# Optimization experiments

Hardware: AMD Instinct MI355X
Metric: run time of the kernel (lower is better)

The kernel has to match this reference:

```python
import jax, jax.numpy as jnp
import numpy as np

NUM_COARSE = 1024

def sqdist(a, b):
    # a: [..., N, 3], b: [..., M, 3] -> [..., N, M] squared euclidean distances
    d = (jnp.sum(a * a, -1)[..., :, None] + jnp.sum(b * b, -1)[..., None, :]
         - 2.0 * jnp.einsum('...nd,...md->...nm', a, b))
    return jnp.maximum(d, 0.0)

def fps_idx(pts, n_samples):
    # pts: [N, 3]; farthest point sampling starting from index 0 (pn2 convention)
    d0 = jnp.sum((pts - pts[0]) ** 2, -1)  # [N]
    def step(dists, _):
        idx = jnp.argmax(dists)
        d = jnp.sum((pts - pts[idx]) ** 2, -1)
        return jnp.minimum(dists, d), idx
    _, idxs = jax.lax.scan(step, d0, None, length=n_samples - 1)
    return jnp.concatenate([jnp.zeros((1,), jnp.int32), idxs.astype(jnp.int32)])

def emd_dist(x, y, eps, iters):
    # x, y: [n, 3] equal-cardinality clouds. Approximate optimal assignment via
    # log-domain entropic OT (eps = regularization, iters = iterations), then
    # per-point squared distance to the matched point (as in the auction EMD kernel).
    n = x.shape[0]
    C = sqdist(x, y)                       # [n, n]
    Cs = jax.lax.stop_gradient(C)          # assignment is a constant wrt grads
    loga = -jnp.log(jnp.float32(n))
    def step(f, _):
        g = -eps * jax.nn.logsumexp((f[:, None] - Cs) / eps + loga, axis=0)
        f = -eps * jax.nn.logsumexp((g[None, :] - Cs) / eps + loga, axis=1)
        return f, None
    f, _ = jax.lax.scan(step, jnp.zeros((n,), Cs.dtype), None, length=iters)
    g = -eps * jax.nn.logsumexp((f[:, None] - Cs) / eps + loga, axis=0)
    assign = jnp.argmax(f[:, None] + g[None, :] - Cs, axis=1)  # [n]
    return jnp.take_along_axis(C, assign[:, None], axis=1)[:, 0]

def chamfer(a, b):
    # a: [B, N, 3], b: [B, M, 3] -> per-point min squared dists ([B,N], [B,M])
    C = sqdist(a, b)
    return jnp.min(C, axis=2), jnp.min(C, axis=1)

def setup_inputs() -> dict:
    key = jax.random.key(0)
    k1, k2, k3 = jax.random.split(key, 3)
    return {
        'output1': jax.random.uniform(k1, (4, NUM_COARSE, 3), jnp.float32),
        'output2': jax.random.uniform(k2, (4, 4096, 3), jnp.float32),
        'gt': jax.random.uniform(k3, (4, 4096, 3), jnp.float32),
        'eps': jnp.float32(0.005),
        'iters': 10,
    }

def reference(output1, output2, gt, eps, iters):
    gt = gt[:, :, :3]
    # --- EMD branch ---
    idx = jax.vmap(lambda p: fps_idx(p, NUM_COARSE))(gt)            # [B, num_coarse]
    gt_fps = jnp.take_along_axis(gt, idx[:, :, None], axis=1)       # [B, num_coarse, 3]
    d1 = jax.vmap(lambda x, y: emd_dist(x, y, eps, iters))(output1, gt_fps)
    emd1 = jnp.sqrt(d1).mean(1)
    d2 = jax.vmap(lambda x, y: emd_dist(x, y, eps, iters))(output2, gt)
    emd2 = jnp.sqrt(d2).mean(1)
    # --- Chamfer branch ---
    d11, d12 = chamfer(gt, output1)
    cd_p1 = (jnp.sqrt(d11).mean(1) + jnp.sqrt(d12).mean(1)) / 2
    cd_t1 = d11.mean(1) + d12.mean(1)
    d21, d22 = chamfer(gt, output2)
    cd_p2 = (jnp.sqrt(d21).mean(1) + jnp.sqrt(d22).mean(1)) / 2
    cd_t2 = d21.mean(1) + d22.mean(1)
    return (output1, output2, emd1, emd2, cd_p1, cd_p2, cd_t1, cd_t2)
```

## Files before the change

### kernel.cpp

```cpp
#include <hip/hip_runtime.h>
#include <math.h>


#define LOG2E 1.4426950408889634f
#define LN2   0.6931471805599453f
#define NEGBIG -3.0e38f

#define SY2(b) ((b) * 512)
#define SYF(b) (2048 + (b) * 16)
#define SYD(b) (2112 + (b) * 16)

typedef float f32x2 __attribute__((ext_vector_type(2)));

#if __has_builtin(__builtin_amdgcn_exp2f)
__device__ __forceinline__ float fexp2(float x) { return __builtin_amdgcn_exp2f(x); }
#else
__device__ __forceinline__ float fexp2(float x) { return exp2f(x); }
#endif

__device__ __forceinline__ float dist_rn(float x, float y, float z,
                                         float qx, float qy, float qz) {
  float dx = __fsub_rn(x, qx), dy = __fsub_rn(y, qy), dz = __fsub_rn(z, qz);
  return __fadd_rn(__fadd_rn(__fmul_rn(dx, dx), __fmul_rn(dy, dy)),
                   __fmul_rn(dz, dz));
}

__device__ __forceinline__ f32x2 dist2_rn(f32x2 x, f32x2 y, f32x2 z,
                                          float qx, float qy, float qz) {
#pragma clang fp contract(off)
  f32x2 dx = x - qx;
  f32x2 dy = y - qy;
  f32x2 dz = z - qz;
  f32x2 xx = dx * dx;
  f32x2 yy = dy * dy;
  f32x2 zz = dz * dz;
  return (xx + yy) + zz;
}

struct FpsS {
  float4 sq[4096];
  unsigned long long xch[4][2];
  int sIdx[64];
};
struct WorkS {
  float4 ldsRow[256];
  float4 ldsC[1024];
  float ldsG2[1024];
  float red[8];
};
struct Emd1S {
  float4 rowsO[1024];
  float4 rowsG[1024];
  float2 part[2][16][64];
  float g2[1024];
  float red[8];
};
union SmemAll {
  FpsS f;
  WorkS w;
  Emd1S e;
  float pad_force_one_block_per_cu[21504];
};

struct UniArgs {
  const float* gt;
  const float* epsP;
  const float4 *o1P4, *o2P4, *gtP4;
  float4* gfP4;
  float2 *gpart2, *fpart2, *apart2;
  unsigned long long* vecT;
  unsigned* sync;
  float* out;
  int NC2, BPB;
};

__device__ __forceinline__ void bar_signal(unsigned* slot, unsigned val) {
  __syncthreads();
  if (threadIdx.x == 0)
    __hip_atomic_store(slot, val, __ATOMIC_RELEASE, __HIP_MEMORY_SCOPE_AGENT);
}
template <int SLP>
__device__ __forceinline__ void bar_waitall(const unsigned* base, int n,
                                            unsigned target) {
  if (threadIdx.x < 64) {
    int l = threadIdx.x;
    for (;;) {
      unsigned v = (l < n)
                       ? __hip_atomic_load(base + l * 16, __ATOMIC_RELAXED,
                                           __HIP_MEMORY_SCOPE_AGENT)
                       : target;
      if (__all((int)(v >= target))) break;
      __builtin_amdgcn_s_sleep(SLP);
    }
    if (l == 0)
      (void)__hip_atomic_load(base, __ATOMIC_ACQUIRE, __HIP_MEMORY_SCOPE_AGENT);
  }
  __syncthreads();
}

__device__ __forceinline__ float blockRedSum(float v, float* red4) {
#pragma unroll
  for (int m = 32; m; m >>= 1) v += __shfl_xor(v, m, 64);
  int lane = threadIdx.x & 63, wid = threadIdx.x >> 6;
  __syncthreads();
  if (lane == 0) red4[wid] = v;
  __syncthreads();
  float s = 0.0f;
  if (threadIdx.x == 0) {
#pragma unroll
    for (int w = 0; w < 4; ++w) s += red4[w];
  }
  return s;
}

__device__ __forceinline__ void poll4(const unsigned long long* v, int tid,
                                      unsigned want, float* w0, float* w1,
                                      float* w2, float* w3) {
  unsigned long long p0, p1, p2, p3;
  for (;;) {
    p0 = __hip_atomic_load(v + tid, __ATOMIC_RELAXED, __HIP_MEMORY_SCOPE_AGENT);
    p1 = __hip_atomic_load(v + tid + 256, __ATOMIC_RELAXED, __HIP_MEMORY_SCOPE_AGENT);
    p2 = __hip_atomic_load(v + tid + 512, __ATOMIC_RELAXED, __HIP_MEMORY_SCOPE_AGENT);
    p3 = __hip_atomic_load(v + tid + 768, __ATOMIC_RELAXED, __HIP_MEMORY_SCOPE_AGENT);
    if ((unsigned)(p0 >> 32) >= want && (unsigned)(p1 >> 32) >= want &&
        (unsigned)(p2 >> 32) >= want && (unsigned)(p3 >> 32) >= want)
      break;
    __builtin_amdgcn_s_sleep(1);
  }
  *w0 = __uint_as_float((unsigned)p0);
  *w1 = __uint_as_float((unsigned)p1);
  *w2 = __uint_as_float((unsigned)p2);
  *w3 = __uint_as_float((unsigned)p3);
}

__device__ __forceinline__ void fma_burst(float* a) {
#pragma unroll
  for (int i = 0; i < 64; ++i) {
    a[0] = fmaf(a[0], 1.0000001f, 1.0e-6f);
    a[1] = fmaf(a[1], 1.0000001f, 1.0e-6f);
    a[2] = fmaf(a[2], 1.0000001f, 1.0e-6f);
    a[3] = fmaf(a[3], 1.0000001f, 1.0e-6f);
  }
}

__device__ void warm_spin(const UniArgs& A) {
  float a[4] = {(float)(threadIdx.x + 1), 1.5f, 2.5f, 3.5f};
  const unsigned* sy = A.sync;
  for (;;) {
    unsigned d0 = __hip_atomic_load(sy + SYD(0), __ATOMIC_RELAXED, __HIP_MEMORY_SCOPE_AGENT);
    unsigned d1 = __hip_atomic_load(sy + SYD(1), __ATOMIC_RELAXED, __HIP_MEMORY_SCOPE_AGENT);
    unsigned d2 = __hip_atomic_load(sy + SYD(2), __ATOMIC_RELAXED, __HIP_MEMORY_SCOPE_AGENT);
    unsigned d3 = __hip_atomic_load(sy + SYD(3), __ATOMIC_RELAXED, __HIP_MEMORY_SCOPE_AGENT);
    if ((d0 & d1 & d2 & d3) != 0u) break;
    fma_burst(a);
  }
  asm volatile("" ::"v"(a[0]), "v"(a[1]), "v"(a[2]), "v"(a[3]));
}

__device__ void warm_wait1(const unsigned* slot, unsigned target) {
  float a[4] = {(float)(threadIdx.x + 1), 1.5f, 2.5f, 3.5f};
  for (;;) {
    unsigned v = __hip_atomic_load(slot, __ATOMIC_RELAXED, __HIP_MEMORY_SCOPE_AGENT);
    if (v >= target) break;
    fma_burst(a);
  }
  asm volatile("" ::"v"(a[0]), "v"(a[1]), "v"(a[2]), "v"(a[3]));
  if (threadIdx.x == 0)
    (void)__hip_atomic_load(slot, __ATOMIC_ACQUIRE, __HIP_MEMORY_SCOPE_AGENT);
  __syncthreads();
}

__global__ __launch_bounds__(256) void prep_kernel(
    const float* __restrict__ o1, const float* __restrict__ o2,
    const float* __restrict__ gt, const float* __restrict__ epsP,
    float4* __restrict__ o1P4, float4* __restrict__ o2P4,
    float4* __restrict__ gtP4) {
  int id = blockIdx.x * 256 + threadIdx.x;
  float eps = *epsP;
  float se = (1.0f / eps) * LOG2E;
  float kxy = sqrtf(se + se);
  const float* src;
  float4* dst;
  if (id < 4096) { src = o1 + 3 * id; dst = o1P4 + id; }
  else if (id < 20480) { int p = id - 4096; src = o2 + 3 * p; dst = o2P4 + p; }
  else { int p = id - 20480; src = gt + 3 * p; dst = gtP4 + p; }
  float x = src[0], y = src[1], z = src[2];
  float xx = x * x + y * y + z * z;
  *dst = make_float4(kxy * x, kxy * y, kxy * z, xx * se);
}

template <int NC>
__device__ __forceinline__ float finalize_w(const float2* __restrict__ part,
                                            int gi, int stride, float nloga2) {
  float2 pp[NC];
#pragma unroll
  for (int c = 0; c < NC; ++c) pp[c] = part[c * stride + gi];
  float m = pp[0].x;
#pragma unroll
  for (int c = 1; c < NC; ++c) m = fmaxf(m, pp[c].x);
  float s = 0.0f;
#pragma unroll
  for (int c = 0; c < NC; ++c) s += pp[c].y * fexp2(pp[c].x - m);
  return nloga2 - (m + __log2f(s));
}

template <int NC>
__device__ void pass2_job(int b, int cb, int ch, const float4* __restrict__ rowP,
                          const float4* __restrict__ colP,
                          const float2* __restrict__ vpart,
                          float2* __restrict__ dst, float4* ldsRow) {
  const int CH = 4096 / NC;
  int tid = threadIdx.x;
  int gj = b * 4096 + cb * 2048 + tid;
  float cx[8], cy[8], cz[8];
#pragma unroll
  for (int c = 0; c < 8; ++c) {
    float4 cp = colP[gj + (c << 8)];
    cx[c] = cp.x; cy[c] = cp.y; cz[c] = cp.z;
  }
  float M[8], S[8];
#pragma unroll
  for (int c = 0; c < 8; ++c) { M[c] = NEGBIG; S[c] = 0.0f; }
  int r0 = ch * CH;
  for (int t0 = 0; t0 < CH; t0 += 256) {
    __syncthreads();
    {
      int gi = b * 4096 + r0 + t0 + tid;
      float4 rp = rowP[gi];
      float w = vpart ? finalize_w<NC>(vpart, gi, 16384, 12.0f) : -rp.w;
      ldsRow[tid] = make_float4(rp.x, rp.y, rp.z, w);
    }
    __syncthreads();
#pragma unroll 1
    for (int r = 0; r < 256; r += 8) {
      float4 q[8];
#pragma unroll
      for (int u = 0; u < 8; ++u) q[u] = ldsRow[r + u];
#pragma unroll
      for (int c = 0; c < 8; ++c) {
        float t[8];
#pragma unroll
        for (int u = 0; u < 8; ++u)
          t[u] = fmaf(cx[c], q[u].x, fmaf(cy[c], q[u].y, fmaf(cz[c], q[u].z, q[u].w)));
        float cm = fmaxf(fmaxf(fmaxf(t[0], t[1]), fmaxf(t[2], t[3])),
                         fmaxf(fmaxf(t[4], t[5]), fmaxf(t[6], t[7])));
        float nM = fmaxf(M[c], cm);
        float s8 = ((fexp2(t[0] - nM) + fexp2(t[1] - nM)) +
                    (fexp2(t[2] - nM) + fexp2(t[3] - nM))) +
                   ((fexp2(t[4] - nM) + fexp2(t[5] - nM)) +
                    (fexp2(t[6] - nM) + fexp2(t[7] - nM)));
        S[c] = fmaf(S[c], fexp2(M[c] - nM), s8);
        M[c] = nM;
      }
    }
  }
#pragma unroll
  for (int c = 0; c < 8; ++c)
    dst[ch * 16384 + gj + (c << 8)] = make_float2(M[c], S[c]);
}

__device__ void cham_job(const float4* __restrict__ aP, const float4* __restrict__ bP,
                         int Na, int Nb, float* outP, float* outT,
                         float scaleP, float scaleT, int b, int rb,
                         WorkS& w, const float* epsP) {
  int tid = threadIdx.x;
  int i0 = rb * 512 + tid, i1 = i0 + 256;
  float4 a0 = aP[b * Na + i0], a1 = aP[b * Na + i1];
  float m0 = 3.0e38f, m1 = 3.0e38f;
  for (int t0 = 0; t0 < Nb; t0 += 1024) {
    __syncthreads();
    for (int t = tid; t < 1024; t += 256) w.ldsC[t] = bP[b * Nb + t0 + t];
    __syncthreads();
#pragma unroll 4
    for (int t = 0; t < 1024; ++t) {
      float4 q = w.ldsC[t];
      float c0 = fmaf(-a0.z, q.z, fmaf(-a0.y, q.y, fmaf(-a0.x, q.x, q.w + a0.w)));
      float c1 = fmaf(-a1.z, q.z, fmaf(-a1.y, q.y, fmaf(-a1.x, q.x, q.w + a1.w)));
      m0 = fminf(m0, c0);
      m1 = fminf(m1, c1);
    }
  }
  float eps = *epsP;
  float inv_se = eps * LN2;
  float d0 = fmaxf(0.0f, m0 * inv_se), d1 = fmaxf(0.0f, m1 * inv_se);
  float s1 = blockRedSum(sqrtf(d0) + sqrtf(d1), w.red);
  float s2 = blockRedSum(d0 + d1, w.red);
  if (tid == 0) {
    atomicAdd(outP, s1 * scaleP);
    atomicAdd(outT, s2 * scaleT);
  }
}

__device__ void chamfer_worker(int g, const UniArgs& A, WorkS& w) {
  for (int cj = g; cj < 104; cj += 88) {
    if (cj < 32) {
      cham_job(A.gtP4, A.o2P4, 4096, 4096, A.out + 61452 + (cj >> 3),
               A.out + 61460 + (cj >> 3), 1.0f / 8192.0f, 1.0f / 4096.0f,
               cj >> 3, cj & 7, w, A.epsP);
    } else if (cj < 64) {
      int j = cj - 32;
      cham_job(A.o2P4, A.gtP4, 4096, 4096, A.out + 61452 + (j >> 3),
               A.out + 61460 + (j >> 3), 1.0f / 8192.0f, 1.0f / 4096.0f,
               j >> 3, j & 7, w, A.epsP);
    } else if (cj < 96) {
      int j = cj - 64;
      cham_job(A.gtP4, A.o1P4, 4096, 1024, A.out + 61448 + (j >> 3),
               A.out + 61456 + (j >> 3), 1.0f / 8192.0f, 1.0f / 4096.0f,
               j >> 3, j & 7, w, A.epsP);
    } else {
      int j = cj - 96;
      cham_job(A.o1P4, A.gtP4, 1024, 4096, A.out + 61448 + (j >> 1),
               A.out + 61456 + (j >> 1), 1.0f / 2048.0f, 1.0f / 1024.0f,
               j >> 1, j & 1, w, A.epsP);
    }
  }
}

template <int NC>
__device__ void assign2_job(int b, int cc, int rb, const UniArgs& A, WorkS& w) {
  int tid = threadIdx.x;
  __syncthreads();
  for (int t = tid; t < 1024; t += 256) {
    int gjc = b * 4096 + cc * 1024 + t;
    float wv = finalize_w<NC>(A.gpart2, gjc, 16384, 12.0f);
    float4 qp = A.gtP4[gjc];
    w.ldsC[t] = make_float4(qp.x, qp.y, qp.z, wv);
    w.ldsG2[t] = wv + qp.w;
  }
  __syncthreads();
#pragma unroll
  for (int rr = 0; rr < 2; ++rr) {
    int gi = b * 4096 + rb * 512 + (rr << 8) + tid;
    float4 rp = A.o2P4[gi];
    float rx = rp.x, ry = rp.y, rz = rp.z, xw = rp.w;
    float bW = NEGBIG;
    int bj = 0;
    for (int t = 0; t < 1024; ++t) {
      float4 q = w.ldsC[t];
      float W = fmaf(rz, q.z, fmaf(ry, q.y, fmaf(rx, q.x, q.w - xw)));
      W = fminf(W, w.ldsG2[t]);
      if (W > bW) { bW = W; bj = cc * 1024 + t; }
    }
    A.apart2[cc * 16384 + gi] = make_float2(bW, __int_as_float(bj));
  }
}

__device__ void combine2_job(int b, int rb, const UniArgs& A, WorkS& w) {
  int tid = threadIdx.x;
  int gi = b * 4096 + (rb << 8) + tid;
  float bW = NEGBIG;
  int bj = 0;
#pragma unroll
  for (int c = 0; c < 4; ++c) {
    float2 p = A.apart2[c * 16384 + gi];
    if (p.x > bW) { bW = p.x; bj = __float_as_int(p.y); }
  }
  float eps = *A.epsP;
  float inv_se = eps * LN2;
  float4 rp = A.o2P4[gi];
  float4 qp = A.gtP4[b * 4096 + bj];
  float dotp = rp.x * qp.x + rp.y * qp.y + rp.z * qp.z;
  float d = fmaxf(0.0f, (rp.w + qp.w - dotp) * inv_se);
  float s = blockRedSum(sqrtf(d), w.red);
  if (tid == 0) atomicAdd(A.out + 61444 + b, s * (1.0f / 4096.0f));
}

__device__ void fps_role(const UniArgs& A, int b, FpsS& f) {
  int tid = threadIdx.x;
  const float* base = A.gt + b * 12288;
  for (int t = tid; t < 4096; t += 256) {
    float x = base[3 * t], y = base[3 * t + 1], z = base[3 * t + 2];
    f.sq[t] = make_float4(x, y, z, x * x + y * y + z * z);
  }
  if (tid < 8) ((unsigned long long*)f.xch)[tid] = 0ull;
  if (tid == 0) f.sIdx[0] = 0;
  __syncthreads();
  float eps = *A.epsP;
  float se = (1.0f / eps) * LOG2E;
  float kxy = sqrtf(se + se);
  float4 p0 = f.sq[0];
  f32x2 PX[8], PY[8], PZ[8];
  float d[16];
#pragma unroll
  for (int k = 0; k < 16; ++k) {
    float4 p = f.sq[tid + (k << 8)];
    PX[k >> 1][k & 1] = p.x;
    PY[k >> 1][k & 1] = p.y;
    PZ[k >> 1][k & 1] = p.z;
    d[k] = dist_rn(p.x, p.y, p.z, p0.x, p0.y, p0.z);
  }
  int lane = tid & 63, w = tid >> 6;
  float qx = p0.x, qy = p0.y, qz = p0.z;
  unsigned long long* xmine = &f.xch[w][0];

#define DPPSTEP(C)                                                             \
  {                                                                            \
    unsigned ov = (unsigned)__builtin_amdgcn_update_dpp(0, (int)bvu, C, 0xf,  \
                                                        0xf, true);           \
    int oi = __builtin_amdgcn_update_dpp(0, bi, C, 0xf, 0xf, true);           \
    bool t = (ov > bvu) || ((ov == bvu) && ((unsigned)oi < (unsigned)bi));    \
    bvu = t ? ov : bvu;                                                        \
    bi = t ? oi : bi;                                                          \
  }
#define XCOMB(G)                                                               \
  {                                                                            \
    unsigned _v = (unsigned)((G) >> 32);                                       \
    int _i = (int)((unsigned)(G) & 0xFFFu);                                    \
    if (_v > bv2 || (_v == bv2 && _i < bi2)) { bv2 = _v; bi2 = _i; }          \
  }

#pragma unroll 1
  for (int s = 1; s < 1024; ++s) {
    if ((s & 63) == 0 && tid < 64) {
      int idx = f.sIdx[tid];
      float4 p = f.sq[idx];
      A.gfP4[(b << 10) + (s - 64) + tid] =
          make_float4(kxy * p.x, kxy * p.y, kxy * p.z, p.w * se);
    }
    float tv[8]; int ti[8];
#pragma unroll
    for (int i = 0; i < 8; ++i) {
      f32x2 nn = dist2_rn(PX[i], PY[i], PZ[i], qx, qy, qz);
      float n0 = fminf(d[2 * i], nn[0]);
      float n1 = fminf(d[2 * i + 1], nn[1]);
      d[2 * i] = n0;
      d[2 * i + 1] = n1;
      bool t = n1 > n0;
      tv[i] = t ? n1 : n0;
      ti[i] = tid + ((t ? (2 * i + 1) : (2 * i)) << 8);
    }
    float uv[4]; int ui[4];
#pragma unroll
    for (int i = 0; i < 4; ++i) {
      bool t = tv[2 * i + 1] > tv[2 * i];
      uv[i] = t ? tv[2 * i + 1] : tv[2 * i];
      ui[i] = t ? ti[2 * i + 1] : ti[2 * i];
    }
    bool tA = uv[1] > uv[0];
    float vA = tA ? uv[1] : uv[0]; int iA = tA ? ui[1] : ui[0];
    bool tB = uv[3] > uv[2];
    float vB = tB ? uv[3] : uv[2]; int iB = tB ? ui[3] : ui[2];
    bool tC = vB > vA;
    float bv = tC ? vB : vA; int bi = tC ? iB : iA;
    unsigned bvu = __float_as_uint(bv);
    DPPSTEP(0xB1)
    DPPSTEP(0x4E)
    DPPSTEP(0x141)
    DPPSTEP(0x140)
    unsigned r0v = (unsigned)__builtin_amdgcn_readlane((int)bvu, 0);
    int r0i = __builtin_amdgcn_readlane(bi, 0);
    unsigned r1v = (unsigned)__builtin_amdgcn_readlane((int)bvu, 16);
    int r1i = __builtin_amdgcn_readlane(bi, 16);
    unsigned r2v = (unsigned)__builtin_amdgcn_readlane((int)bvu, 32);
    int r2i = __builtin_amdgcn_readlane(bi, 32);
    unsigned r3v = (unsigned)__builtin_amdgcn_readlane((int)bvu, 48);
    int r3i = __builtin_amdgcn_readlane(bi, 48);
    bool tP = (r1v > r0v) || (r1v == r0v && r1i < r0i);
    unsigned pv = tP ? r1v : r0v; int pi = tP ? r1i : r0i;
    bool tQ = (r3v > r2v) || (r3v == r2v && r3i < r2i);
    unsigned qv = tQ ? r3v : r2v; int qi = tQ ? r3i : r2i;
    bool tR = (qv > pv) || (qv == pv && qi < pi);
    unsigned wv = tR ? qv : pv; int wi = tR ? qi : pi;
    int par = s & 1;
    unsigned tagw = (unsigned)(s & 1023);
    unsigned long long mine = ((unsigned long long)wv << 32) |
                              ((unsigned long long)tagw << 16) |
                              (unsigned long long)(unsigned)wi;
    if (lane == 0)
      __hip_atomic_store(xmine + par, mine, __ATOMIC_RELAXED,
                         __HIP_MEMORY_SCOPE_WORKGROUP);
    float4 mq = f.sq[wi];
    unsigned long long g1, g2, g3;
    for (;;) {
      g1 = __hip_atomic_load(&f.xch[(w + 1) & 3][par], __ATOMIC_RELAXED,
                             __HIP_MEMORY_SCOPE_WORKGROUP);
      g2 = __hip_atomic_load(&f.xch[(w + 2) & 3][par], __ATOMIC_RELAXED,
                             __HIP_MEMORY_SCOPE_WORKGROUP);
      g3 = __hip_atomic_load(&f.xch[(w + 3) & 3][par], __ATOMIC_RELAXED,
                             __HIP_MEMORY_SCOPE_WORKGROUP);
      if ((((unsigned)(g1 >> 16) & 1023u) == tagw) &
          (((unsigned)(g2 >> 16) & 1023u) == tagw) &
          (((unsigned)(g3 >> 16) & 1023u) == tagw))
        break;
    }
    unsigned bv2 = wv; int bi2 = wi;
    XCOMB(g1) XCOMB(g2) XCOMB(g3)
    float4 q;
    if (bv2 == wv && bi2 == wi) q = mq;
    else q = f.sq[bi2];
    qx = q.x; qy = q.y; qz = q.z;
    if (tid == 0) f.sIdx[s & 63] = bi2;
  }
#undef DPPSTEP
#undef XCOMB
  if (tid < 64) {
    int idx = f.sIdx[tid];
    float4 p = f.sq[idx];
    A.gfP4[(b << 10) + 960 + tid] =
        make_float4(kxy * p.x, kxy * p.y, kxy * p.z, p.w * se);
  }
  bar_signal(A.sync + SYF(b), 1u);
}

__device__ void emd1_role(int eb, int chunk, const UniArgs& A, Emd1S& m) {
  int tid = threadIdx.x;
  warm_wait1(A.sync + SYF(eb), 1u);
  for (int t = tid; t < 1024; t += 256) {
    float4 p = A.o1P4[eb * 1024 + t];
    m.rowsO[t] = make_float4(p.x, p.y, p.z, -p.w);
    m.rowsG[t] = A.gfP4[eb * 1024 + t];
  }
  int lane = tid & 63, rl = tid >> 6;
  int col = chunk * 64 + lane;
  float4 cG = A.gfP4[eb * 1024 + col];
  float4 cO = A.o1P4[eb * 1024 + col];
  unsigned long long* gv = A.vecT + (eb << 10);
  unsigned long long* fv = A.vecT + 4096 + (eb << 10);
  __syncthreads();

  for (int s = 1; s <= 21; ++s) {
    int odd = s & 1, par = s & 1;
    if (s >= 2) {
      const unsigned long long* v = odd ? fv : gv;
      float4* rows = odd ? m.rowsO : m.rowsG;
      unsigned want = (unsigned)(s - 1);
      int rbase = rl * 256 + lane;
      unsigned long long p0, p1, p2, p3;
      for (;;) {
        p0 = __hip_atomic_load(v + rbase, __ATOMIC_RELAXED, __HIP_MEMORY_SCOPE_AGENT);
        p1 = __hip_atomic_load(v + rbase + 64, __ATOMIC_RELAXED, __HIP_MEMORY_SCOPE_AGENT);
        p2 = __hip_atomic_load(v + rbase + 128, __ATOMIC_RELAXED, __HIP_MEMORY_SCOPE_AGENT);
        p3 = __hip_atomic_load(v + rbase + 192, __ATOMIC_RELAXED, __HIP_MEMORY_SCOPE_AGENT);
        if ((unsigned)(p0 >> 32) >= want && (unsigned)(p1 >> 32) >= want &&
            (unsigned)(p2 >> 32) >= want && (unsigned)(p3 >> 32) >= want)
          break;
        __builtin_amdgcn_s_sleep(1);
      }
      rows[rbase].w = __uint_as_float((unsigned)p0);
      rows[rbase + 64].w = __uint_as_float((unsigned)p1);
      rows[rbase + 128].w = __uint_as_float((unsigned)p2);
      rows[rbase + 192].w = __uint_as_float((unsigned)p3);
    }
    const float4* rows = odd ? m.rowsO : m.rowsG;
    float cx = odd ? cG.x : cO.x;
    float cy = odd ? cG.y : cO.y;
    float cz = odd ? cG.z : cO.z;
#pragma unroll 1
    for (int k = 0; k < 4; ++k) {
      int ch = rl * 4 + k;
      float M = NEGBIG, S = 0.0f;
      int r0 = ch * 64;
#pragma unroll 1
      for (int r = 0; r < 64; r += 8) {
        float4 qq[8];
#pragma unroll
        for (int u = 0; u < 8; ++u) qq[u] = rows[r0 + r + u];
        float t8[8];
#pragma unroll
        for (int u = 0; u < 8; ++u)
          t8[u] = fmaf(cx, qq[u].x, fmaf(cy, qq[u].y, fmaf(cz, qq[u].z, qq[u].w)));
        float cm = fmaxf(fmaxf(fmaxf(t8[0], t8[1]), fmaxf(t8[2], t8[3])),
                         fmaxf(fmaxf(t8[4], t8[5]), fmaxf(t8[6], t8[7])));
        float nM = fmaxf(M, cm);
        float s8 = ((fexp2(t8[0] - nM) + fexp2(t8[1] - nM)) +
                    (fexp2(t8[2] - nM) + fexp2(t8[3] - nM))) +
                   ((fexp2(t8[4] - nM) + fexp2(t8[5] - nM)) +
                    (fexp2(t8[6] - nM) + fexp2(t8[7] - nM)));
        S = fmaf(S, fexp2(M - nM), s8);
        M = nM;
      }
      m.part[par][ch][lane] = make_float2(M, S);
    }
    __syncthreads();
    if (tid < 64) {
      float2 pp[16];
#pragma unroll
      for (int c = 0; c < 16; ++c) pp[c] = m.part[par][c][tid];
      float mm = pp[0].x;
#pragma unroll
      for (int c = 1; c < 16; ++c) mm = fmaxf(mm, pp[c].x);
      float ss = 0.0f;
#pragma unroll
      for (int c = 0; c < 16; ++c) ss += pp[c].y * fexp2(pp[c].x - mm);
      float wq = 10.0f - (mm + __log2f(ss));
      unsigned long long pk = ((unsigned long long)(unsigned)s << 32) |
                              (unsigned long long)__float_as_uint(wq);
      __hip_atomic_store((odd ? gv : fv) + col, pk, __ATOMIC_RELAXED,
                         __HIP_MEMORY_SCOPE_AGENT);
    }
  }
  __syncthreads();

  {
    float w0, w1, w2, w3;
    poll4(gv, tid, 21u, &w0, &w1, &w2, &w3);
    float4 qp0 = A.gfP4[eb * 1024 + tid];
    float4 qp1 = A.gfP4[eb * 1024 + tid + 256];
    float4 qp2 = A.gfP4[eb * 1024 + tid + 512];
    float4 qp3 = A.gfP4[eb * 1024 + tid + 768];
    m.rowsG[tid] = make_float4(qp0.x, qp0.y, qp0.z, w0);
    m.g2[tid] = w0 + qp0.w;
    m.rowsG[tid + 256] = make_float4(qp1.x, qp1.y, qp1.z, w1);
    m.g2[tid + 256] = w1 + qp1.w;
    m.rowsG[tid + 512] = make_float4(qp2.x, qp2.y, qp2.z, w2);
    m.g2[tid + 512] = w2 + qp2.w;
    m.rowsG[tid + 768] = make_float4(qp3.x, qp3.y, qp3.z, w3);
    m.g2[tid + 768] = w3 + qp3.w;
  }
  __syncthreads();
  float eps = *A.epsP;
  float inv_se = eps * LN2;
  int rw = tid & 63, qc = tid >> 6;
  int gi = eb * 1024 + chunk * 64 + rw;
  float4 rp = A.o1P4[gi];
  float rx = rp.x, ry = rp.y, rz = rp.z, xw = rp.w;
  float bW = NEGBIG;
  int bj = 0;
  int t0 = qc * 256;
  for (int t = t0; t < t0 + 256; ++t) {
    float4 q = m.rowsG[t];
    float W = fmaf(rz, q.z, fmaf(ry, q.y, fmaf(rx, q.x, q.w - xw)));
    W = fminf(W, m.g2[t]);
    if (W > bW) { bW = W; bj = t; }
  }
  m.part[0][qc][rw] = make_float2(bW, __int_as_float(bj));
  __syncthreads();
  if (tid < 64) {
    float2 p0 = m.part[0][0][tid];
    float vb = p0.x;
    int vj = __float_as_int(p0.y);
#pragma unroll
    for (int c = 1; c < 4; ++c) {
      float2 p = m.part[0][c][tid];
      if (p.x > vb) { vb = p.x; vj = __float_as_int(p.y); }
    }
    float4 qp = A.gfP4[eb * 1024 + vj];
    float dotp = rp.x * qp.x + rp.y * qp.y + rp.z * qp.z;
    float dd = fmaxf(0.0f, (rp.w + qp.w - dotp) * inv_se);
    float v = sqrtf(dd);
#pragma unroll
    for (int mk = 32; mk; mk >>= 1) v += __shfl_xor(v, mk, 64);
    if (tid == 0) atomicAdd(A.out + 61440 + eb, v * (1.0f / 1024.0f));
  }
  if (chunk == 0) bar_signal(A.sync + SYD(eb), 1u);
}

__global__ __launch_bounds__(256, 1) void uni_kernel(UniArgs A) {
  __shared__ SmemAll sm;
  int bid = blockIdx.x;
  if (bid < 4) {
    fps_role(A, bid, sm.f);
    return;
  }
  int e = bid - 4;
  int W = 4 * A.BPB;
  if (e < W) {
    int b = e / A.BPB, rest = e % A.BPB;
    int cb = rest / A.NC2, ch = rest % A.NC2;
    unsigned* slots = A.sync + SY2(b);
    for (int s = 1; s <= 21; ++s) {
      const float4 *rowP, *colP;
      const float2* vp;
      float2* dst;
      if (s & 1) { rowP = A.o2P4; colP = A.gtP4; vp = (s == 1) ? nullptr : A.fpart2; dst = A.gpart2; }
      else       { rowP = A.gtP4; colP = A.o2P4; vp = A.gpart2; dst = A.fpart2; }
      if (A.NC2 == 16) pass2_job<16>(b, cb, ch, rowP, colP, vp, dst, sm.w.ldsRow);
      else             pass2_job<8>(b, cb, ch, rowP, colP, vp, dst, sm.w.ldsRow);
      bar_signal(slots + rest * 16, (unsigned)s);
      bar_waitall<16>(slots, A.BPB, (unsigned)s);
    }
    for (int j = rest; j < 32; j += A.BPB) {
      int cc = j >> 3, rb = j & 7;
      if (A.NC2 == 16) assign2_job<16>(b, cc, rb, A, sm.w);
      else             assign2_job<8>(b, cc, rb, A, sm.w);
    }
    bar_signal(slots + rest * 16, 22u);
    bar_waitall<4>(slots, A.BPB, 22u);
    if (rest < 16) combine2_job(b, rest, A, sm.w);
    if (e < 64) warm_spin(A);
    return;
  }
  int g = e - W;
  chamfer_worker(g, A, sm.w);
  if (g < 64) {
    emd1_role(g >> 4, g & 15, A, sm.e);
  }
}

extern "C" void kernel_launch(void* const* d_in, const int* in_sizes, int n_in,
                              void* d_out, int out_size, void* d_ws, size_t ws_size,
                              hipStream_t stream) {
  (void)in_sizes; (void)n_in; (void)out_size;
  const float* o1 = (const float*)d_in[0];
  const float* o2 = (const float*)d_in[1];
  const float* gt = (const float*)d_in[2];
  const float* epsP = (const float*)d_in[3];
  float* out = (float*)d_out;
  float* ws = (float*)d_ws;

  int NC2 = 16;
  {
    size_t need16 = (size_t)(4096 + 16384 + 16384 + 65536 + 65536 + 16384 +
                             2 * (16 * 32768)) * 4;
    if (ws_size < need16) NC2 = 8;
  }
  size_t off = 0;
  unsigned* syncp = (unsigned*)(ws + off); off += 4096;
  unsigned long long* vecT = (unsigned long long*)(ws + off); off += 16384;
  float4* o1P4 = (float4*)(ws + off); off += 16384;
  float4* o2P4 = (float4*)(ws + off); off += 65536;
  float4* gtP4 = (float4*)(ws + off); off += 65536;
  float4* gfP4 = (float4*)(ws + off); off += 16384;
  float2* gpart2 = (float2*)(ws + off); off += (size_t)NC2 * 32768;
  float2* fpart2 = (float2*)(ws + off); off += (size_t)NC2 * 32768;
  float2* apart2 = fpart2;

  (void)hipMemcpyAsync(out, o1, 12288 * sizeof(float), hipMemcpyDeviceToDevice, stream);
  (void)hipMemcpyAsync(out + 12288, o2, 49152 * sizeof(float), hipMemcpyDeviceToDevice, stream);
  (void)hipMemsetAsync(out + 61440, 0, 24 * sizeof(float), stream);
  (void)hipMemsetAsync(syncp, 0, (4096 + 16384) * sizeof(float), stream);

  prep_kernel<<<144, 256, 0, stream>>>(o1, o2, gt, epsP, o1P4, o2P4, gtP4);

  UniArgs A;
  A.gt = gt; A.epsP = epsP;
  A.o1P4 = o1P4; A.o2P4 = o2P4; A.gtP4 = gtP4; A.gfP4 = gfP4;
  A.gpart2 = gpart2; A.fpart2 = fpart2; A.apart2 = apart2;
  A.vecT = vecT;
  A.sync = syncp; A.out = out;
  A.NC2 = NC2; A.BPB = 2 * NC2;
  int grid = 4 + 4 * A.BPB + 88;
  uni_kernel<<<grid, 256, 0, stream>>>(A);
}
```

Baseline: 1.085 ms.

## Run farthest-point sampling for two batches per block, interleaving their chains

```diff
diff --git a/kernel.cpp b/kernel.cpp
--- a/kernel.cpp
+++ b/kernel.cpp
@@ -37,10 +37,13 @@
   return (xx + yy) + zz;
 }
 
-struct FpsS {
+struct FpsP {
   float4 sq[4096];
   unsigned long long xch[4][2];
   int sIdx[64];
+};
+struct FpsS {
+  FpsP p[2];
 };
 struct WorkS {
   float4 ldsRow[256];
@@ -59,7 +62,6 @@
   FpsS f;
   WorkS w;
   Emd1S e;
-  float pad_force_one_block_per_cu[21504];
 };
 
 struct UniArgs {
@@ -365,34 +367,36 @@
   if (tid == 0) atomicAdd(A.out + 61444 + b, s * (1.0f / 4096.0f));
 }
 
-__device__ void fps_role(const UniArgs& A, int b, FpsS& f) {
-  int tid = threadIdx.x;
-  const float* base = A.gt + b * 12288;
-  for (int t = tid; t < 4096; t += 256) {
-    float x = base[3 * t], y = base[3 * t + 1], z = base[3 * t + 2];
-    f.sq[t] = make_float4(x, y, z, x * x + y * y + z * z);
-  }
-  if (tid < 8) ((unsigned long long*)f.xch)[tid] = 0ull;
-  if (tid == 0) f.sIdx[0] = 0;
-  __syncthreads();
-  float eps = *A.epsP;
-  float se = (1.0f / eps) * LOG2E;
-  float kxy = sqrtf(se + se);
-  float4 p0 = f.sq[0];
-  f32x2 PX[8], PY[8], PZ[8];
-  float d[16];
-#pragma unroll
-  for (int k = 0; k < 16; ++k) {
-    float4 p = f.sq[tid + (k << 8)];
-    PX[k >> 1][k & 1] = p.x;
-    PY[k >> 1][k & 1] = p.y;
-    PZ[k >> 1][k & 1] = p.z;
-    d[k] = dist_rn(p.x, p.y, p.z, p0.x, p0.y, p0.z);
-  }
-  int lane = tid & 63, w = tid >> 6;
-  float qx = p0.x, qy = p0.y, qz = p0.z;
-  unsigned long long* xmine = &f.xch[w][0];
-
+__device__ __forceinline__ void leaf_reduce(f32x2* PX, f32x2* PY, f32x2* PZ,
+                                            f32x2* D, float qx, float qy,
+                                            float qz, int tid, unsigned& wvO,
+                                            int& wiO) {
+  float tv[8]; int ti[8];
+#pragma unroll
+  for (int i = 0; i < 8; ++i) {
+    f32x2 nn = dist2_rn(PX[i], PY[i], PZ[i], qx, qy, qz);
+    float n0 = fminf(D[i][0], nn[0]);
+    float n1 = fminf(D[i][1], nn[1]);
+    D[i][0] = n0;
+    D[i][1] = n1;
+    bool t = n1 > n0;
+    tv[i] = t ? n1 : n0;
+    ti[i] = tid + ((t ? (2 * i + 1) : (2 * i)) << 8);
+  }
+  float uv[4]; int ui[4];
+#pragma unroll
+  for (int i = 0; i < 4; ++i) {
+    bool t = tv[2 * i + 1] > tv[2 * i];
+    uv[i] = t ? tv[2 * i + 1] : tv[2 * i];
+    ui[i] = t ? ti[2 * i + 1] : ti[2 * i];
+  }
+  bool tA = uv[1] > uv[0];
+  float vA = tA ? uv[1] : uv[0]; int iA = tA ? ui[1] : ui[0];
+  bool tB = uv[3] > uv[2];
+  float vB = tB ? uv[3] : uv[2]; int iB = tB ? ui[3] : ui[2];
+  bool tC = vB > vA;
+  float bv = tC ? vB : vA; int bi = tC ? iB : iA;
+  unsigned bvu = __float_as_uint(bv);
 #define DPPSTEP(C)                                                             \
   {                                                                            \
     unsigned ov = (unsigned)__builtin_amdgcn_update_dpp(0, (int)bvu, C, 0xf,  \
@@ -402,104 +406,155 @@
     bvu = t ? ov : bvu;                                                        \
     bi = t ? oi : bi;                                                          \
   }
+  DPPSTEP(0xB1)
+  DPPSTEP(0x4E)
+  DPPSTEP(0x141)
+  DPPSTEP(0x140)
+#undef DPPSTEP
+  unsigned r0v = (unsigned)__builtin_amdgcn_readlane((int)bvu, 0);
+  int r0i = __builtin_amdgcn_readlane(bi, 0);
+  unsigned r1v = (unsigned)__builtin_amdgcn_readlane((int)bvu, 16);
+  int r1i = __builtin_amdgcn_readlane(bi, 16);
+  unsigned r2v = (unsigned)__builtin_amdgcn_readlane((int)bvu, 32);
+  int r2i = __builtin_amdgcn_readlane(bi, 32);
+  unsigned r3v = (unsigned)__builtin_amdgcn_readlane((int)bvu, 48);
+  int r3i = __builtin_amdgcn_readlane(bi, 48);
+  bool tP = (r1v > r0v) || (r1v == r0v && r1i < r0i);
+  unsigned pv = tP ? r1v : r0v; int pi = tP ? r1i : r0i;
+  bool tQ = (r3v > r2v) || (r3v == r2v && r3i < r2i);
+  unsigned qv = tQ ? r3v : r2v; int qi = tQ ? r3i : r2i;
+  bool tR = (qv > pv) || (qv == pv && qi < pi);
+  wvO = tR ? qv : pv;
+  wiO = tR ? qi : pi;
+}
+
+__device__ __forceinline__ int poll_sel(unsigned long long (*xch)[2], int w,
+                                        int par, unsigned tagw, unsigned wv,
+                                        int wi) {
+  unsigned long long g1, g2, g3;
+  for (;;) {
+    g1 = __hip_atomic_load(&xch[(w + 1) & 3][par], __ATOMIC_RELAXED,
+                           __HIP_MEMORY_SCOPE_WORKGROUP);
+    g2 = __hip_atomic_load(&xch[(w + 2) & 3][par], __ATOMIC_RELAXED,
+                           __HIP_MEMORY_SCOPE_WORKGROUP);
+    g3 = __hip_atomic_load(&xch[(w + 3) & 3][par], __ATOMIC_RELAXED,
+                           __HIP_MEMORY_SCOPE_WORKGROUP);
+    if ((((unsigned)(g1 >> 16) & 1023u) == tagw) &
+        (((unsigned)(g2 >> 16) & 1023u) == tagw) &
+        (((unsigned)(g3 >> 16) & 1023u) == tagw))
+      break;
+  }
+  unsigned bv2 = wv; int bi2 = wi;
 #define XCOMB(G)                                                               \
   {                                                                            \
     unsigned _v = (unsigned)((G) >> 32);                                       \
     int _i = (int)((unsigned)(G) & 0xFFFu);                                    \
     if (_v > bv2 || (_v == bv2 && _i < bi2)) { bv2 = _v; bi2 = _i; }          \
   }
+  XCOMB(g1) XCOMB(g2) XCOMB(g3)
+#undef XCOMB
+  return bi2;
+}
+
+__device__ void fps_role2(const UniArgs& A, int b0, FpsS& f) {
+  int tid = threadIdx.x;
+#pragma unroll
+  for (int h = 0; h < 2; ++h) {
+    const float* base = A.gt + (b0 + h) * 12288;
+    for (int t = tid; t < 4096; t += 256) {
+      float x = base[3 * t], y = base[3 * t + 1], z = base[3 * t + 2];
+      f.p[h].sq[t] = make_float4(x, y, z, x * x + y * y + z * z);
+    }
+  }
+  if (tid < 8) {
+    ((unsigned long long*)f.p[0].xch)[tid] = 0ull;
+    ((unsigned long long*)f.p[1].xch)[tid] = 0ull;
+  }
+  if (tid == 0) { f.p[0].sIdx[0] = 0; f.p[1].sIdx[0] = 0; }
+  __syncthreads();
+  float eps = *A.epsP;
+  float se = (1.0f / eps) * LOG2E;
+  float kxy = sqrtf(se + se);
+  int lane = tid & 63, w = tid >> 6;
+
+  float4 p0A = f.p[0].sq[0];
+  float4 p0B = f.p[1].sq[0];
+  f32x2 PXA[8], PYA[8], PZA[8], DA[8];
+  f32x2 PXB[8], PYB[8], PZB[8], DB[8];
+#pragma unroll
+  for (int k = 0; k < 16; ++k) {
+    float4 pa = f.p[0].sq[tid + (k << 8)];
+    PXA[k >> 1][k & 1] = pa.x;
+    PYA[k >> 1][k & 1] = pa.y;
+    PZA[k >> 1][k & 1] = pa.z;
+    float4 pb = f.p[1].sq[tid + (k << 8)];
+    PXB[k >> 1][k & 1] = pb.x;
+    PYB[k >> 1][k & 1] = pb.y;
+    PZB[k >> 1][k & 1] = pb.z;
+  }
+#pragma unroll
+  for (int i = 0; i < 8; ++i) {
+    DA[i] = dist2_rn(PXA[i], PYA[i], PZA[i], p0A.x, p0A.y, p0A.z);
+    DB[i] = dist2_rn(PXB[i], PYB[i], PZB[i], p0B.x, p0B.y, p0B.z);
+  }
+  float qxA = p0A.x, qyA = p0A.y, qzA = p0A.z;
+  float qxB = p0B.x, qyB = p0B.y, qzB = p0B.z;
 
 #pragma unroll 1
   for (int s = 1; s < 1024; ++s) {
     if ((s & 63) == 0 && tid < 64) {
-      int idx = f.sIdx[tid];
-      float4 p = f.sq[idx];
-      A.gfP4[(b << 10) + (s - 64) + tid] =
-          make_float4(kxy * p.x, kxy * p.y, kxy * p.z, p.w * se);
-    }
-    float tv[8]; int ti[8];
-#pragma unroll
-    for (int i = 0; i < 8; ++i) {
-      f32x2 nn = dist2_rn(PX[i], PY[i], PZ[i], qx, qy, qz);
-      float n0 = fminf(d[2 * i], nn[0]);
-      float n1 = fminf(d[2 * i + 1], nn[1]);
-      d[2 * i] = n0;
-      d[2 * i + 1] = n1;
-      bool t = n1 > n0;
-      tv[i] = t ? n1 : n0;
-      ti[i] = tid + ((t ? (2 * i + 1) : (2 * i)) << 8);
-    }
-    float uv[4]; int ui[4];
-#pragma unroll
-    for (int i = 0; i < 4; ++i) {
-      bool t = tv[2 * i + 1] > tv[2 * i];
-      uv[i] = t ? tv[2 * i + 1] : tv[2 * i];
-      ui[i] = t ? ti[2 * i + 1] : ti[2 * i];
-    }
-    bool tA = uv[1] > uv[0];
-    float vA = tA ? uv[1] : uv[0]; int iA = tA ? ui[1] : ui[0];
-    bool tB = uv[3] > uv[2];
-    float vB = tB ? uv[3] : uv[2]; int iB = tB ? ui[3] : ui[2];
-    bool tC = vB > vA;
-    float bv = tC ? vB : vA; int bi = tC ? iB : iA;
-    unsigned bvu = __float_as_uint(bv);
-    DPPSTEP(0xB1)
-    DPPSTEP(0x4E)
-    DPPSTEP(0x141)
-    DPPSTEP(0x140)
-    unsigned r0v = (unsigned)__builtin_amdgcn_readlane((int)bvu, 0);
-    int r0i = __builtin_amdgcn_readlane(bi, 0);
-    unsigned r1v = (unsigned)__builtin_amdgcn_readlane((int)bvu, 16);
-    int r1i = __builtin_amdgcn_readlane(bi, 16);
-    unsigned r2v = (unsigned)__builtin_amdgcn_readlane((int)bvu, 32);
-    int r2i = __builtin_amdgcn_readlane(bi, 32);
-    unsigned r3v = (unsigned)__builtin_amdgcn_readlane((int)bvu, 48);
-    int r3i = __builtin_amdgcn_readlane(bi, 48);
-    bool tP = (r1v > r0v) || (r1v == r0v && r1i < r0i);
-    unsigned pv = tP ? r1v : r0v; int pi = tP ? r1i : r0i;
-    bool tQ = (r3v > r2v) || (r3v == r2v && r3i < r2i);
-    unsigned qv = tQ ? r3v : r2v; int qi = tQ ? r3i : r2i;
-    bool tR = (qv > pv) || (qv == pv && qi < pi);
-    unsigned wv = tR ? qv : pv; int wi = tR ? qi : pi;
+      int ia = f.p[0].sIdx[tid];
+      float4 pa = f.p[0].sq[ia];
+      A.gfP4[(b0 << 10) + (s - 64) + tid] =
+          make_float4(kxy * pa.x, kxy * pa.y, kxy * pa.z, pa.w * se);
+      int ib = f.p[1].sIdx[tid];
+      float4 pb = f.p[1].sq[ib];
+      A.gfP4[((b0 + 1) << 10) + (s - 64) + tid] =
+          make_float4(kxy * pb.x, kxy * pb.y, kxy * pb.z, pb.w * se);
+    }
     int par = s & 1;
     unsigned tagw = (unsigned)(s & 1023);
-    unsigned long long mine = ((unsigned long long)wv << 32) |
-                              ((unsigned long long)tagw << 16) |
-                              (unsigned long long)(unsigned)wi;
-    if (lane == 0)
-      __hip_atomic_store(xmine + par, mine, __ATOMIC_RELAXED,
+    unsigned wvA; int wiA;
+    leaf_reduce(PXA, PYA, PZA, DA, qxA, qyA, qzA, tid, wvA, wiA);
+    if (lane == 0) {
+      unsigned long long mine = ((unsigned long long)wvA << 32) |
+                                ((unsigned long long)tagw << 16) |
+                                (unsigned long long)(unsigned)wiA;
+      __hip_atomic_store(&f.p[0].xch[w][par], mine, __ATOMIC_RELAXED,
                          __HIP_MEMORY_SCOPE_WORKGROUP);
-    float4 mq = f.sq[wi];
-    unsigned long long g1, g2, g3;
-    for (;;) {
-      g1 = __hip_atomic_load(&f.xch[(w + 1) & 3][par], __ATOMIC_RELAXED,
-                             __HIP_MEMORY_SCOPE_WORKGROUP);
-      g2 = __hip_atomic_load(&f.xch[(w + 2) & 3][par], __ATOMIC_RELAXED,
-                             __HIP_MEMORY_SCOPE_WORKGROUP);
-      g3 = __hip_atomic_load(&f.xch[(w + 3) & 3][par], __ATOMIC_RELAXED,
-                             __HIP_MEMORY_SCOPE_WORKGROUP);
-      if ((((unsigned)(g1 >> 16) & 1023u) == tagw) &
-          (((unsigned)(g2 >> 16) & 1023u) == tagw) &
-          (((unsigned)(g3 >> 16) & 1023u) == tagw))
-        break;
-    }
-    unsigned bv2 = wv; int bi2 = wi;
-    XCOMB(g1) XCOMB(g2) XCOMB(g3)
-    float4 q;
-    if (bv2 == wv && bi2 == wi) q = mq;
-    else q = f.sq[bi2];
-    qx = q.x; qy = q.y; qz = q.z;
-    if (tid == 0) f.sIdx[s & 63] = bi2;
-  }
-#undef DPPSTEP
-#undef XCOMB
+    }
+    unsigned wvB; int wiB;
+    leaf_reduce(PXB, PYB, PZB, DB, qxB, qyB, qzB, tid, wvB, wiB);
+    if (lane == 0) {
+      unsigned long long mine = ((unsigned long long)wvB << 32) |
+                                ((unsigned long long)tagw << 16) |
+                                (unsigned long long)(unsigned)wiB;
+      __hip_atomic_store(&f.p[1].xch[w][par], mine, __ATOMIC_RELAXED,
+                         __HIP_MEMORY_SCOPE_WORKGROUP);
+    }
+    int biA = poll_sel(f.p[0].xch, w, par, tagw, wvA, wiA);
+    float4 qA = f.p[0].sq[biA];
+    int biB = poll_sel(f.p[1].xch, w, par, tagw, wvB, wiB);
+    float4 qB = f.p[1].sq[biB];
+    qxA = qA.x; qyA = qA.y; qzA = qA.z;
+    qxB = qB.x; qyB = qB.y; qzB = qB.z;
+    if (tid == 0) {
+      f.p[0].sIdx[s & 63] = biA;
+      f.p[1].sIdx[s & 63] = biB;
+    }
+  }
   if (tid < 64) {
-    int idx = f.sIdx[tid];
-    float4 p = f.sq[idx];
-    A.gfP4[(b << 10) + 960 + tid] =
-        make_float4(kxy * p.x, kxy * p.y, kxy * p.z, p.w * se);
-  }
-  bar_signal(A.sync + SYF(b), 1u);
+    int ia = f.p[0].sIdx[tid];
+    float4 pa = f.p[0].sq[ia];
+    A.gfP4[(b0 << 10) + 960 + tid] =
+        make_float4(kxy * pa.x, kxy * pa.y, kxy * pa.z, pa.w * se);
+    int ib = f.p[1].sIdx[tid];
+    float4 pb = f.p[1].sq[ib];
+    A.gfP4[((b0 + 1) << 10) + 960 + tid] =
+        make_float4(kxy * pb.x, kxy * pb.y, kxy * pb.z, pb.w * se);
+  }
+  bar_signal(A.sync + SYF(b0), 1u);
+  bar_signal(A.sync + SYF(b0 + 1), 1u);
 }
 
 __device__ void emd1_role(int eb, int chunk, const UniArgs& A, Emd1S& m) {
@@ -648,10 +703,11 @@
 __global__ __launch_bounds__(256, 1) void uni_kernel(UniArgs A) {
   __shared__ SmemAll sm;
   int bid = blockIdx.x;
-  if (bid < 4) {
-    fps_role(A, bid, sm.f);
+  if (bid < 2) {
+    fps_role2(A, bid * 2, sm.f);
     return;
   }
+  if (bid < 4) return;
   int e = bid - 4;
   int W = 4 * A.BPB;
   if (e < W) {
```

Measured after the change: 2.035 ms. 87.5% more time.
